# Performance work log

Hardware: AMD Instinct MI355X
Metric: run time of the kernel (lower is better)

Reference implementation:

```python
import jax, jax.numpy as jnp
import numpy as np

B, CIN, X, Y = 4, 3, 128, 128
D, L, DEPTH, OUT = 64, 8, 4, 1
GRID_RANGE = 1.0
LN_EPS = 1e-5
YR = Y // 2 + 1


def _build_phi_f():
    # 1D Hilbert-matrix eigenbases along each axis, outer product, then rfft2.
    def top_eigvecs(n):
        i = np.arange(n)
        Z = 1.0 / (i[:, None] + i[None, :] + 1.0)  # Hilbert matrix, float64
        w, V = np.linalg.eigh(Z)
        idx = np.argsort(-w)[:L]
        return V.T[idx]  # (L, n)

    Vx = top_eigvecs(X)
    Vy = top_eigvecs(Y)
    phi = Vx[:, :, None] * Vy[:, None, :]  # (L, X, Y) separable eigenfunctions
    Phi_f = np.fft.rfft2(phi, s=(X, Y))  # (L, X, YR)
    return jnp.asarray(Phi_f, dtype=jnp.complex64)


def setup_inputs() -> dict:
    key = jax.random.key(0)
    ks = jax.random.split(key, 16)
    u = lambda k, shape, bound: jax.random.uniform(k, shape, jnp.float32, -bound, bound)
    inv = 1.0 / np.sqrt(D)
    inp = {
        "x": jax.random.normal(ks[0], (B, CIN, X, Y), jnp.float32),
        "Phi_f": _build_phi_f(),  # constant buffer
        "lift_w": u(ks[1], (D, CIN + 2), 1.0 / np.sqrt(CIN + 2)),
        "lift_b": u(ks[2], (D,), 1.0 / np.sqrt(CIN + 2)),
        "Theta": u(ks[3], (DEPTH, L, D, D), 1.0 / D),  # kaiming_uniform(a=sqrt(5)) ~ U(-1/d, 1/d)
        "glu_val_w": u(ks[4], (DEPTH, D, D), inv),
        "glu_val_b": u(ks[5], (DEPTH, D), inv),
        "glu_gate_w": u(ks[6], (DEPTH, D, D), inv),
        "glu_gate_b": u(ks[7], (DEPTH, D), inv),
        "ln_g": jnp.ones((DEPTH, D), jnp.float32),
        "ln_b": jnp.zeros((DEPTH, D), jnp.float32),
        "head_w": u(ks[8], (OUT, D), inv),
        "head_b": u(ks[9], (OUT,), inv),
    }
    return inp


def _stu_layer(h, Phi_f, Theta, vw, vb, gw, gb, g, b):
    # LayerNorm over channel dim (torch LayerNorm on channels-last view)
    ht = jnp.transpose(h, (0, 2, 3, 1))  # (B, X, Y, D)
    mu = jnp.mean(ht, axis=-1, keepdims=True)
    var = jnp.var(ht, axis=-1, keepdims=True)
    zt = (ht - mu) * jax.lax.rsqrt(var + LN_EPS) * g + b
    z = jnp.transpose(zt, (0, 3, 1, 2))  # (B, D, X, Y)

    Xf = jnp.fft.rfftn(z, axes=(-2, -1))  # (B, D, X, YR) complex
    Uf = Xf[:, :, None, :, :] * jnp.conj(Phi_f)[None, None]  # (B, D, L, X, YR)
    U = jnp.fft.irfftn(Uf, s=(X, Y), axes=(-2, -1))  # (B, D, L, X, Y)
    # einsum('bdlxy,lhd->bhlxy') followed by sum over l, fused:
    S = jnp.einsum("bdlxy,lhd->bhxy", U, Theta)

    V = jnp.einsum("bhxy,oh->boxy", S, vw) + vb[None, :, None, None]
    G = jax.nn.sigmoid(jnp.einsum("bhxy,oh->boxy", S, gw) + gb[None, :, None, None])
    return h + V * G


def reference(x, Phi_f, lift_w, lift_b, Theta, glu_val_w, glu_val_b,
              glu_gate_w, glu_gate_b, ln_g, ln_b, head_w, head_b):
    bsz = x.shape[0]
    # add_2d_grid: append yy, xx coordinate channels
    ys = jnp.linspace(0.0, GRID_RANGE, X, dtype=x.dtype)
    xs = jnp.linspace(0.0, GRID_RANGE, Y, dtype=x.dtype)
    yy, xx = jnp.meshgrid(ys, xs, indexing="ij")
    yy = jnp.broadcast_to(yy[None, None], (bsz, 1, X, Y))
    xx = jnp.broadcast_to(xx[None, None], (bsz, 1, X, Y))
    h = jnp.concatenate([x, yy, xx], axis=1)  # (B, CIN+2, X, Y)

    # LocalLift2D with kernel_size=1 -> pointwise conv
    h = jnp.einsum("bcxy,dc->bdxy", h, lift_w) + lift_b[None, :, None, None]

    for i in range(DEPTH):
        h = _stu_layer(h, Phi_f, Theta[i], glu_val_w[i], glu_val_b[i],
                       glu_gate_w[i], glu_gate_b[i], ln_g[i], ln_b[i])

    y = jnp.einsum("bdxy,od->boxy", h, head_w) + head_b[None, :, None, None]
    return y
```

## Files before the change

### kernel.cpp

```cpp
#include <hip/hip_runtime.h>
#include <math.h>
#include <string.h>


#define NXY 16384

#define OFF_V       16
#define OFF_MC      1040
#define OFF_THETAA  132112
#define OFF_AG      263184
#define OFF_Z       295952
#define OFF_H       4490256
#define OFF_P       8684560
#define WS_NEED_F   25461776ULL

typedef short short8 __attribute__((ext_vector_type(8)));
typedef float float4m __attribute__((ext_vector_type(4)));

__device__ __forceinline__ unsigned short bf_rn(float f) {
    unsigned u = __float_as_uint(f);
    u += 0x7fffu + ((u >> 16) & 1u);
    return (unsigned short)(u >> 16);
}
__device__ __forceinline__ float bf_tof(unsigned short s) {
    return __uint_as_float(((unsigned)s) << 16);
}

__global__ void poison_out(float* out) { out[0] = 1e9f; }


static float vhost[1024];

static void host_hilbert_topk(float* outv) {
    static double Vs[8][128];
    static double W[8][128];
    double recip[256];
    for (int i = 0; i < 256; i++) recip[i] = 1.0 / (double)(i + 1);
    for (int j = 0; j < 8; j++)
        for (int i = 0; i < 128; i++) Vs[j][i] = recip[i + j];
    for (int outer = 0; outer < 25; outer++) {
        for (int half = 0; half < 2; half++) {
            for (int j = 0; j < 8; j++)
                for (int i = 0; i < 128; i++) {
                    double s = 0.0;
                    for (int k = 0; k < 128; k++) s += Vs[j][k] * recip[i + k];
                    W[j][i] = s;
                }
            memcpy(Vs, W, sizeof(Vs));
        }
        for (int j = 0; j < 8; j++) {
            for (int p = 0; p < j; p++) {
                double d = 0.0;
                for (int i = 0; i < 128; i++) d += Vs[j][i] * Vs[p][i];
                for (int i = 0; i < 128; i++) Vs[j][i] -= d * Vs[p][i];
            }
            double nn = 0.0;
            for (int i = 0; i < 128; i++) nn += Vs[j][i] * Vs[j][i];
            double inv = 1.0 / sqrt(nn);
            for (int i = 0; i < 128; i++) Vs[j][i] *= inv;
        }
    }
    for (int j = 0; j < 8; j++)
        for (int i = 0; i < 128; i++) outv[j * 128 + i] = (float)Vs[j][i];
}

namespace {
struct VInit {
    VInit() { host_hilbert_topk(vhost); }
};
VInit vinit_once;
}

__global__ void build_mct(const float* __restrict__ v, unsigned short* __restrict__ McT) {
    int l = blockIdx.y;
    int idx = blockIdx.x * 256 + threadIdx.x;
    int r = idx >> 7, k = idx & 127;
    McT[l * 16384 + idx] = bf_rn(v[l * 128 + ((k - r) & 127)]);
}


__global__ void build_thetaAHL(const float* __restrict__ Theta, unsigned short* __restrict__ ThA) {
    int i = blockIdx.x * 256 + threadIdx.x;
    int k = i & 127; int r = i >> 7;
    int m = r & 127; r >>= 7;
    int tile = r & 3; int dep = r >> 2;
    int l2 = m >> 6, hch = m & 63, d = k & 63;
    float f = Theta[(((dep * 8 + tile * 2 + l2) * 64) + hch) * 64 + d];
    unsigned short hb = bf_rn(f);
    ThA[i] = (k < 64) ? hb : bf_rn(f - bf_tof(hb));
}

__global__ void build_AG(const float* __restrict__ vw, const float* __restrict__ gw,
                         float* __restrict__ AG) {
    int i = blockIdx.x * 256 + threadIdx.x;
    int m = i & 127; int r = i >> 7; int h = r & 63; int dep = r >> 6;
    int o = m >> 1;
    const float* W = (m & 1) ? gw : vw;
    AG[i] = W[(dep * 64 + o) * 64 + h];
}


__global__ void lift_kernel(const float* __restrict__ x, const float* __restrict__ lw,
                            const float* __restrict__ lb, float* __restrict__ h) {
    __shared__ float w[320];
    __shared__ float bsm[64];
    int tid = threadIdx.x;
    for (int i = tid; i < 320; i += 256) w[i] = lw[i];
    if (tid < 64) bsm[tid] = lb[tid];
    __syncthreads();
    int b = blockIdx.y;
    int xy = blockIdx.x * 256 + tid;
    int xi = xy >> 7, yi = xy & 127;
    float c0 = x[(size_t)(b * 3 + 0) * NXY + xy];
    float c1 = x[(size_t)(b * 3 + 1) * NXY + xy];
    float c2 = x[(size_t)(b * 3 + 2) * NXY + xy];
    float yyv = xi * (1.0f / 127.0f), xxv = yi * (1.0f / 127.0f);
    for (int d = 0; d < 64; d++) {
        float acc = bsm[d] + w[d * 5] * c0 + w[d * 5 + 1] * c1 + w[d * 5 + 2] * c2
                  + w[d * 5 + 3] * yyv + w[d * 5 + 4] * xxv;
        h[(size_t)(b * 64 + d) * NXY + xy] = acc;
    }
}

__global__ void ln_kernel(const float* __restrict__ h, const float* __restrict__ g,
                          const float* __restrict__ bb, unsigned short* __restrict__ zT) {
    int x = blockIdx.x, b = blockIdx.y, y = threadIdx.x;
    __shared__ float gs[64], bs[64];
    if (y < 64) gs[y] = g[y]; else bs[y - 64] = bb[y - 64];
    __syncthreads();
    const float* hp = h + (size_t)b * (64 * NXY) + x * 128 + y;
    float v[64];
    float sum = 0.f;
#pragma unroll
    for (int d = 0; d < 64; d++) { v[d] = hp[(size_t)d * NXY]; sum += v[d]; }
    float mu = sum * (1.0f / 64.0f);
    float vs = 0.f;
#pragma unroll
    for (int d = 0; d < 64; d++) { float t = v[d] - mu; vs += t * t; }
    float inv = rsqrtf(vs * (1.0f / 64.0f) + 1e-5f);
    unsigned short t[64];
#pragma unroll
    for (int d = 0; d < 64; d++) t[d] = bf_rn((v[d] - mu) * inv * gs[d] + bs[d]);
    unsigned short* zp = zT + ((size_t)b * NXY + x * 128 + y) * 64;
#pragma unroll
    for (int i = 0; i < 8; i++) {
        uint4 pk;
        pk.x = (unsigned)t[8 * i + 0] | ((unsigned)t[8 * i + 1] << 16);
        pk.y = (unsigned)t[8 * i + 2] | ((unsigned)t[8 * i + 3] << 16);
        pk.z = (unsigned)t[8 * i + 4] | ((unsigned)t[8 * i + 5] << 16);
        pk.w = (unsigned)t[8 * i + 6] | ((unsigned)t[8 * i + 7] << 16);
        *(uint4*)(zp + 8 * i) = pk;
    }
}

__global__ void head_kernel(const float* __restrict__ h, const float* __restrict__ hw,
                            const float* __restrict__ hb, float* __restrict__ out) {
    __shared__ float w[64];
    int tid = threadIdx.x;
    if (tid < 64) w[tid] = hw[tid];
    __syncthreads();
    int b = blockIdx.y;
    int xy = blockIdx.x * 256 + tid;
    float acc = hb[0];
    for (int d = 0; d < 64; d++) acc += h[(size_t)(b * 64 + d) * NXY + xy] * w[d];
    out[(size_t)b * NXY + xy] = acc;
}

__device__ __forceinline__ int sw_idx(int row, int k) {
    return row * 128 + ((((k >> 3) ^ (row & 7)) << 3) | (k & 7));
}


__launch_bounds__(256)
__global__ void k1_mfma(const unsigned short* __restrict__ zT,
                        const unsigned short* __restrict__ ThA,
                        unsigned short* __restrict__ P) {
    __shared__ unsigned short st[16384];
    const int lhtile = blockIdx.x, x = blockIdx.y, b = blockIdx.z;
    const int tid = threadIdx.x;
    const int wid = tid >> 6, lane = tid & 63;
    const int ln15 = lane & 15, q = lane >> 4;
    const int ko = q * 8;
    const unsigned short* Ab = ThA + lhtile * 16384;
    const unsigned short* Bb = zT + ((size_t)b * NXY + x * 128) * 64;

    float4m acc[2][8];
#pragma unroll
    for (int mt = 0; mt < 2; mt++)
#pragma unroll
        for (int nt = 0; nt < 8; nt++) acc[mt][nt] = (float4m){0.f, 0.f, 0.f, 0.f};

#pragma unroll
    for (int k0 = 0; k0 < 128; k0 += 32) {
        short8 a[2];
#pragma unroll
        for (int mt = 0; mt < 2; mt++)
            a[mt] = *(const short8*)(Ab + (wid * 32 + mt * 16 + ln15) * 128 + k0 + ko);
        int d0 = (k0 & 63) + ko;
#pragma unroll
        for (int nt = 0; nt < 8; nt++) {
            int n = nt * 16 + ln15;
            short8 bf = *(const short8*)(Bb + n * 64 + d0);
#pragma unroll
            for (int mt = 0; mt < 2; mt++)
                acc[mt][nt] = __builtin_amdgcn_mfma_f32_16x16x32_bf16(a[mt], bf, acc[mt][nt], 0, 0, 0);
        }
    }
#pragma unroll
    for (int mt = 0; mt < 2; mt++)
#pragma unroll
        for (int nt = 0; nt < 8; nt++) {
            int y = nt * 16 + ln15;
            int r0 = wid * 32 + mt * 16 + q * 4;
            float av[4] = {acc[mt][nt].x, acc[mt][nt].y, acc[mt][nt].z, acc[mt][nt].w};
#pragma unroll
            for (int r = 0; r < 4; r++) st[sw_idx(r0 + r, y)] = bf_rn(av[r]);
        }
    __syncthreads();
    unsigned short* Pb = P + (size_t)(b * 512 + lhtile * 128) * NXY + x * 128;
#pragma unroll
    for (int i = 0; i < 8; i++) {
        int idx = i * 256 + tid;
        int m = idx >> 4, c = idx & 15;
        *(uint4*)(Pb + (size_t)m * NXY + c * 8) = *(const uint4*)&st[sw_idx(m, c * 8)];
    }
}


__launch_bounds__(256)
__global__ void corr2q(unsigned short* __restrict__ P,
                       const unsigned short* __restrict__ McT) {
    __shared__ unsigned short Tt[16384];
    const int hh = blockIdx.x, l = blockIdx.y, b = blockIdx.z;
    unsigned short* plane = P + ((size_t)(b * 8 + l) * 64 + hh) * NXY;
    const unsigned short* Mc = McT + l * 16384;
    const int tid = threadIdx.x;
    const int wid = tid >> 6, lane = tid & 63;
    const int ln15 = lane & 15, q = lane >> 4;
    const int ko = q * 8;

    float4m acc[2][8];
#pragma unroll
    for (int mt = 0; mt < 2; mt++)
#pragma unroll
        for (int nt = 0; nt < 8; nt++) acc[mt][nt] = (float4m){0.f, 0.f, 0.f, 0.f};

#pragma unroll
    for (int k0 = 0; k0 < 128; k0 += 32) {
        short8 a[2];
#pragma unroll
        for (int mt = 0; mt < 2; mt++)
            a[mt] = *(const short8*)(plane + (wid * 32 + mt * 16 + ln15) * 128 + k0 + ko);
#pragma unroll
        for (int nt = 0; nt < 8; nt++) {
            int n = nt * 16 + ln15;
            short8 bf = *(const short8*)(Mc + n * 128 + k0 + ko);
#pragma unroll
            for (int mt = 0; mt < 2; mt++)
                acc[mt][nt] = __builtin_amdgcn_mfma_f32_16x16x32_bf16(a[mt], bf, acc[mt][nt], 0, 0, 0);
        }
    }
#pragma unroll
    for (int mt = 0; mt < 2; mt++)
#pragma unroll
        for (int nt = 0; nt < 8; nt++) {
            int yo = nt * 16 + ln15;
            int x0 = wid * 32 + mt * 16 + q * 4;
            float av[4] = {acc[mt][nt].x, acc[mt][nt].y, acc[mt][nt].z, acc[mt][nt].w};
            unsigned short hs[4];
#pragma unroll
            for (int r = 0; r < 4; r++) hs[r] = bf_rn(av[r]);
            uint2 pk;
            pk.x = (unsigned)hs[0] | ((unsigned)hs[1] << 16);
            pk.y = (unsigned)hs[2] | ((unsigned)hs[3] << 16);
            *(uint2*)&Tt[sw_idx(yo, x0)] = pk;
        }
    __syncthreads();

#pragma unroll
    for (int mt = 0; mt < 2; mt++)
#pragma unroll
        for (int nt = 0; nt < 8; nt++) acc[mt][nt] = (float4m){0.f, 0.f, 0.f, 0.f};
#pragma unroll
    for (int k0 = 0; k0 < 128; k0 += 32) {
        short8 a[2];
#pragma unroll
        for (int mt = 0; mt < 2; mt++)
            a[mt] = *(const short8*)(Mc + (wid * 32 + mt * 16 + ln15) * 128 + k0 + ko);
#pragma unroll
        for (int nt = 0; nt < 8; nt++) {
            int n = nt * 16 + ln15;
            short8 bf = *(const short8*)&Tt[sw_idx(n, k0 + ko)];
#pragma unroll
            for (int mt = 0; mt < 2; mt++)
                acc[mt][nt] = __builtin_amdgcn_mfma_f32_16x16x32_bf16(a[mt], bf, acc[mt][nt], 0, 0, 0);
        }
    }
    __syncthreads();
#pragma unroll
    for (int mt = 0; mt < 2; mt++)
#pragma unroll
        for (int nt = 0; nt < 8; nt++) {
            int y = nt * 16 + ln15;
            int x0 = wid * 32 + mt * 16 + q * 4;
            float av[4] = {acc[mt][nt].x, acc[mt][nt].y, acc[mt][nt].z, acc[mt][nt].w};
#pragma unroll
            for (int r = 0; r < 4; r++) Tt[sw_idx(x0 + r, y)] = bf_rn(av[r]);
        }
    __syncthreads();
#pragma unroll
    for (int i = 0; i < 8; i++) {
        int idx = i * 256 + tid;
        int xr = idx >> 4, c = idx & 15;
        *(uint4*)(plane + xr * 128 + c * 8) = *(const uint4*)&Tt[sw_idx(xr, c * 8)];
    }
}


template <int KTOT, long long BS1, long long PSTR, int NPART>
__launch_bounds__(256)
__global__ void glu_gemm(const float* __restrict__ A0,
                         const unsigned short* __restrict__ B0, long long bsx, long long bsz,
                         float* __restrict__ C0, long long csx, long long csz, long long csm,
                         const float* __restrict__ e_vb, const float* __restrict__ e_gb) {
    constexpr int KS = 16;
    __shared__ float As[KS][132];
    __shared__ float Bs[KS][132];
    const int tid = threadIdx.x;
    const int tm = tid >> 4, tn = tid & 15;
    const int m0 = tm * 8, n0 = tn * 8;
    const float* Ab = A0;
    const unsigned short* Bb = B0 + (long long)blockIdx.x * bsx + (long long)blockIdx.z * bsz;
    float* Cb = C0 + (long long)blockIdx.x * csx + (long long)blockIdx.z * csz;

    float acc[8][8];
#pragma unroll
    for (int i = 0; i < 8; i++)
#pragma unroll
        for (int j = 0; j < 8; j++) acc[i][j] = 0.f;

    for (int k0 = 0; k0 < KTOT; k0 += KS) {
#pragma unroll
        for (int i = 0; i < 2; i++) {
            int idx = tid + i * 256;
            int k = idx >> 5, f4 = (idx & 31) * 4;
            float4 v = *(const float4*)(Ab + (long long)(k0 + k) * 128 + f4);
            *(float4*)&As[k][f4] = v;
        }
#pragma unroll
        for (int i = 0; i < 2; i++) {
            int idx = tid + i * 256;
            int k = idx >> 5, f4 = (idx & 31) * 4;
            const unsigned short* bp = Bb + (long long)(k0 + k) * BS1 + f4;
            float vx = 0.f, vy = 0.f, vz = 0.f, vw = 0.f;
#pragma unroll
            for (int p = 0; p < NPART; p++) {
                uint2 t = *(const uint2*)(bp + (long long)p * PSTR);
                vx += bf_tof((unsigned short)(t.x & 0xffff));
                vy += bf_tof((unsigned short)(t.x >> 16));
                vz += bf_tof((unsigned short)(t.y & 0xffff));
                vw += bf_tof((unsigned short)(t.y >> 16));
            }
            Bs[k][f4] = vx; Bs[k][f4 + 1] = vy; Bs[k][f4 + 2] = vz; Bs[k][f4 + 3] = vw;
        }
        __syncthreads();
#pragma unroll
        for (int kk = 0; kk < KS; kk++) {
            float4 a0 = *(const float4*)&As[kk][m0];
            float4 a1 = *(const float4*)&As[kk][m0 + 4];
            float4 b0 = *(const float4*)&Bs[kk][n0];
            float4 b1 = *(const float4*)&Bs[kk][n0 + 4];
            float av[8] = {a0.x, a0.y, a0.z, a0.w, a1.x, a1.y, a1.z, a1.w};
            float bv[8] = {b0.x, b0.y, b0.z, b0.w, b1.x, b1.y, b1.z, b1.w};
#pragma unroll
            for (int i = 0; i < 8; i++)
#pragma unroll
                for (int j = 0; j < 8; j++) acc[i][j] += av[i] * bv[j];
        }
        __syncthreads();
    }

#pragma unroll
    for (int i = 0; i < 4; i++) {
        int o = (m0 >> 1) + i;
        float vbv = e_vb[o], gbv = e_gb[o];
        float* hp = Cb + (long long)o * csm + n0;
        float4 h0 = *(float4*)hp;
        float4 h1 = *(float4*)(hp + 4);
        float hv[8] = {h0.x, h0.y, h0.z, h0.w, h1.x, h1.y, h1.z, h1.w};
#pragma unroll
        for (int j = 0; j < 8; j++) {
            float V = acc[2 * i][j] + vbv;
            float G = acc[2 * i + 1][j] + gbv;
            float s = 1.0f / (1.0f + expf(-G));
            hv[j] += V * s;
        }
        float4 o0 = {hv[0], hv[1], hv[2], hv[3]};
        float4 o1 = {hv[4], hv[5], hv[6], hv[7]};
        *(float4*)hp = o0;
        *(float4*)(hp + 4) = o1;
    }
}


extern "C" void kernel_launch(void* const* d_in, const int* in_sizes, int n_in,
                              void* d_out, int out_size, void* d_ws, size_t ws_size,
                              hipStream_t stream) {
    const float* x      = (const float*)d_in[0];
    const float* lift_w = (const float*)d_in[2];
    const float* lift_b = (const float*)d_in[3];
    const float* Theta  = (const float*)d_in[4];
    const float* vw     = (const float*)d_in[5];
    const float* vb     = (const float*)d_in[6];
    const float* gw     = (const float*)d_in[7];
    const float* gb     = (const float*)d_in[8];
    const float* ln_g   = (const float*)d_in[9];
    const float* ln_b   = (const float*)d_in[10];
    const float* head_w = (const float*)d_in[11];
    const float* head_b = (const float*)d_in[12];
    float* out = (float*)d_out;
    float* ws = (float*)d_ws;
    (void)in_sizes; (void)n_in; (void)out_size;

    float* v      = ws + OFF_V;
    unsigned short* McT = (unsigned short*)(ws + OFF_MC);
    unsigned short* ThA = (unsigned short*)(ws + OFF_THETAA);
    float* AG     = ws + OFF_AG;
    unsigned short* zT = (unsigned short*)(ws + OFF_Z);
    float* h      = ws + OFF_H;
    unsigned short* P = (unsigned short*)(ws + OFF_P);

    hipMemcpyAsync(v, vhost, sizeof(vhost), hipMemcpyHostToDevice, stream);

    build_mct<<<dim3(64, 8), 256, 0, stream>>>(v, McT);
    build_thetaAHL<<<1024, 256, 0, stream>>>(Theta, ThA);
    build_AG<<<128, 256, 0, stream>>>(vw, gw, AG);

    lift_kernel<<<dim3(64, 4), 256, 0, stream>>>(x, lift_w, lift_b, h);

    for (int dep = 0; dep < 4; dep++) {
        ln_kernel<<<dim3(128, 4), 128, 0, stream>>>(h, ln_g + dep * 64, ln_b + dep * 64, zT);

        k1_mfma<<<dim3(4, 128, 4), 256, 0, stream>>>(zT, ThA + dep * 65536, P);

        corr2q<<<dim3(64, 8, 4), 256, 0, stream>>>(P, McT);

        glu_gemm<64, 16384LL, 1048576LL, 8><<<dim3(128, 1, 4), 256, 0, stream>>>(
            AG + dep * 8192,
            P, 128, 8388608,
            h, 128, 1048576, 16384,
            vb + dep * 64, gb + dep * 64);
    }

    head_kernel<<<dim3(64, 4), 256, 0, stream>>>(h, head_w, head_b, out);

    if (ws_size < WS_NEED_F * 4ULL) {
        poison_out<<<1, 1, 0, stream>>>(out);
    }
}
```

Measured before the change: 611.8 us.

## Fuse LayerNorm into lift and GLU epilogue kernels, removing standalone LN pass

```diff
diff --git a/kernel.cpp b/kernel.cpp
--- a/kernel.cpp
+++ b/kernel.cpp
@@ -100,13 +100,16 @@
 }
 
 
-__global__ void lift_kernel(const float* __restrict__ x, const float* __restrict__ lw,
-                            const float* __restrict__ lb, float* __restrict__ h) {
+__global__ void lift_ln(const float* __restrict__ x, const float* __restrict__ lw,
+                        const float* __restrict__ lb, const float* __restrict__ g0,
+                        const float* __restrict__ b0, float* __restrict__ h,
+                        unsigned short* __restrict__ zT) {
     __shared__ float w[320];
     __shared__ float bsm[64];
+    __shared__ float gs[64], bs[64];
     int tid = threadIdx.x;
     for (int i = tid; i < 320; i += 256) w[i] = lw[i];
-    if (tid < 64) bsm[tid] = lb[tid];
+    if (tid < 64) { bsm[tid] = lb[tid]; gs[tid] = g0[tid]; bs[tid] = b0[tid]; }
     __syncthreads();
     int b = blockIdx.y;
     int xy = blockIdx.x * 256 + tid;
@@ -115,40 +118,32 @@
     float c1 = x[(size_t)(b * 3 + 1) * NXY + xy];
     float c2 = x[(size_t)(b * 3 + 2) * NXY + xy];
     float yyv = xi * (1.0f / 127.0f), xxv = yi * (1.0f / 127.0f);
+    float vv[64];
+    float sum = 0.f;
+#pragma unroll
     for (int d = 0; d < 64; d++) {
         float acc = bsm[d] + w[d * 5] * c0 + w[d * 5 + 1] * c1 + w[d * 5 + 2] * c2
                   + w[d * 5 + 3] * yyv + w[d * 5 + 4] * xxv;
+        vv[d] = acc;
+        sum += acc;
         h[(size_t)(b * 64 + d) * NXY + xy] = acc;
     }
-}
-
-__global__ void ln_kernel(const float* __restrict__ h, const float* __restrict__ g,
-                          const float* __restrict__ bb, unsigned short* __restrict__ zT) {
-    int x = blockIdx.x, b = blockIdx.y, y = threadIdx.x;
-    __shared__ float gs[64], bs[64];
-    if (y < 64) gs[y] = g[y]; else bs[y - 64] = bb[y - 64];
-    __syncthreads();
-    const float* hp = h + (size_t)b * (64 * NXY) + x * 128 + y;
-    float v[64];
-    float sum = 0.f;
-#pragma unroll
-    for (int d = 0; d < 64; d++) { v[d] = hp[(size_t)d * NXY]; sum += v[d]; }
     float mu = sum * (1.0f / 64.0f);
     float vs = 0.f;
 #pragma unroll
-    for (int d = 0; d < 64; d++) { float t = v[d] - mu; vs += t * t; }
+    for (int d = 0; d < 64; d++) { float t = vv[d] - mu; vs += t * t; }
     float inv = rsqrtf(vs * (1.0f / 64.0f) + 1e-5f);
-    unsigned short t[64];
-#pragma unroll
-    for (int d = 0; d < 64; d++) t[d] = bf_rn((v[d] - mu) * inv * gs[d] + bs[d]);
-    unsigned short* zp = zT + ((size_t)b * NXY + x * 128 + y) * 64;
+    unsigned short t16[64];
+#pragma unroll
+    for (int d = 0; d < 64; d++) t16[d] = bf_rn((vv[d] - mu) * inv * gs[d] + bs[d]);
+    unsigned short* zp = zT + ((size_t)b * NXY + xy) * 64;
 #pragma unroll
     for (int i = 0; i < 8; i++) {
         uint4 pk;
-        pk.x = (unsigned)t[8 * i + 0] | ((unsigned)t[8 * i + 1] << 16);
-        pk.y = (unsigned)t[8 * i + 2] | ((unsigned)t[8 * i + 3] << 16);
-        pk.z = (unsigned)t[8 * i + 4] | ((unsigned)t[8 * i + 5] << 16);
-        pk.w = (unsigned)t[8 * i + 6] | ((unsigned)t[8 * i + 7] << 16);
+        pk.x = (unsigned)t16[8 * i + 0] | ((unsigned)t16[8 * i + 1] << 16);
+        pk.y = (unsigned)t16[8 * i + 2] | ((unsigned)t16[8 * i + 3] << 16);
+        pk.z = (unsigned)t16[8 * i + 4] | ((unsigned)t16[8 * i + 5] << 16);
+        pk.w = (unsigned)t16[8 * i + 6] | ((unsigned)t16[8 * i + 7] << 16);
         *(uint4*)(zp + 8 * i) = pk;
     }
 }
@@ -319,13 +314,16 @@
 
 template <int KTOT, long long BS1, long long PSTR, int NPART>
 __launch_bounds__(256)
-__global__ void glu_gemm(const float* __restrict__ A0,
-                         const unsigned short* __restrict__ B0, long long bsx, long long bsz,
-                         float* __restrict__ C0, long long csx, long long csz, long long csm,
-                         const float* __restrict__ e_vb, const float* __restrict__ e_gb) {
+__global__ void glu_ln(const float* __restrict__ A0,
+                       const unsigned short* __restrict__ B0, long long bsx, long long bsz,
+                       float* __restrict__ C0, long long csx, long long csz, long long csm,
+                       const float* __restrict__ e_vb, const float* __restrict__ e_gb,
+                       const float* __restrict__ lngn, const float* __restrict__ lnbn,
+                       unsigned short* __restrict__ zT) {
     constexpr int KS = 16;
     __shared__ float As[KS][132];
     __shared__ float Bs[KS][132];
+    __shared__ float hn[64][129];
     const int tid = threadIdx.x;
     const int tm = tid >> 4, tn = tid & 15;
     const int m0 = tm * 8, n0 = tn * 8;
@@ -394,11 +392,41 @@
             float G = acc[2 * i + 1][j] + gbv;
             float s = 1.0f / (1.0f + expf(-G));
             hv[j] += V * s;
+            hn[o][n0 + j] = hv[j];
         }
         float4 o0 = {hv[0], hv[1], hv[2], hv[3]};
         float4 o1 = {hv[4], hv[5], hv[6], hv[7]};
         *(float4*)hp = o0;
         *(float4*)(hp + 4) = o1;
+    }
+
+    if (lngn != nullptr) {
+        __syncthreads();
+        if (tid < 128) {
+            int xy = tid;
+            float sum = 0.f;
+#pragma unroll
+            for (int d = 0; d < 64; d++) sum += hn[d][xy];
+            float mu = sum * (1.0f / 64.0f);
+            float vs = 0.f;
+#pragma unroll
+            for (int d = 0; d < 64; d++) { float t = hn[d][xy] - mu; vs += t * t; }
+            float inv = rsqrtf(vs * (1.0f / 64.0f) + 1e-5f);
+            unsigned short t16[64];
+#pragma unroll
+            for (int d = 0; d < 64; d++)
+                t16[d] = bf_rn((hn[d][xy] - mu) * inv * lngn[d] + lnbn[d]);
+            unsigned short* zp = zT + ((size_t)blockIdx.z * NXY + blockIdx.x * 128 + xy) * 64;
+#pragma unroll
+            for (int i = 0; i < 8; i++) {
+                uint4 pk;
+                pk.x = (unsigned)t16[8 * i + 0] | ((unsigned)t16[8 * i + 1] << 16);
+                pk.y = (unsigned)t16[8 * i + 2] | ((unsigned)t16[8 * i + 3] << 16);
+                pk.z = (unsigned)t16[8 * i + 4] | ((unsigned)t16[8 * i + 5] << 16);
+                pk.w = (unsigned)t16[8 * i + 6] | ((unsigned)t16[8 * i + 7] << 16);
+                *(uint4*)(zp + 8 * i) = pk;
+            }
+        }
     }
 }
 
@@ -436,20 +464,21 @@
     build_thetaAHL<<<1024, 256, 0, stream>>>(Theta, ThA);
     build_AG<<<128, 256, 0, stream>>>(vw, gw, AG);
 
-    lift_kernel<<<dim3(64, 4), 256, 0, stream>>>(x, lift_w, lift_b, h);
+    lift_ln<<<dim3(64, 4), 256, 0, stream>>>(x, lift_w, lift_b, ln_g, ln_b, h, zT);
 
     for (int dep = 0; dep < 4; dep++) {
-        ln_kernel<<<dim3(128, 4), 128, 0, stream>>>(h, ln_g + dep * 64, ln_b + dep * 64, zT);
-
         k1_mfma<<<dim3(4, 128, 4), 256, 0, stream>>>(zT, ThA + dep * 65536, P);
 
         corr2q<<<dim3(64, 8, 4), 256, 0, stream>>>(P, McT);
 
-        glu_gemm<64, 16384LL, 1048576LL, 8><<<dim3(128, 1, 4), 256, 0, stream>>>(
+        const float* lngn = (dep < 3) ? (ln_g + (dep + 1) * 64) : nullptr;
+        const float* lnbn = (dep < 3) ? (ln_b + (dep + 1) * 64) : nullptr;
+        glu_ln<64, 16384LL, 1048576LL, 8><<<dim3(128, 1, 4), 256, 0, stream>>>(
             AG + dep * 8192,
             P, 128, 8388608,
             h, 128, 1048576, 16384,
-            vb + dep * 64, gb + dep * 64);
+            vb + dep * 64, gb + dep * 64,
+            lngn, lnbn, zT);
     }
 
     head_kernel<<<dim3(64, 4), 256, 0, stream>>>(h, head_w, head_b, out);
```

Result: faster. 591.7 us (-3.3%).
